# Performance work log

Hardware: AMD Instinct MI355X
Metric: run time of the kernel (lower is better)

## Reference

```python
import jax, jax.numpy as jnp
import numpy as np

B, L, T_ENC = 64, 128, 256
C_IN, UNITS, OUT = 256, 512, 128  # state_size == motor_size == UNITS (fully-connected wiring)


def _make_params(key):
    ks = jax.random.split(key, 12)
    def rn(k, shape):
        return jax.random.normal(k, shape, dtype=jnp.float32) / np.sqrt(shape[-1])
    cat = C_IN + UNITS  # CfC cell concatenates [input, hx]
    p = {}
    p["W_dec"] = rn(ks[0], (UNITS, 2 * UNITS))                 # fcn_dec, no bias
    p["W_enc"] = rn(ks[1], (UNITS, UNITS)); p["b_enc"] = jnp.zeros((UNITS,), jnp.float32)
    p["w_score"] = rn(ks[2], (1, UNITS))                       # fcn_score Linear(H,1,bias=False)
    p["W_yattn"] = rn(ks[3], (C_IN, UNITS + C_IN)); p["b_yattn"] = jnp.zeros((C_IN,), jnp.float32)
    p["W_ih"] = rn(ks[4], (4 * UNITS, C_IN)); p["b_ih"] = jnp.zeros((4 * UNITS,), jnp.float32)
    p["W_hh"] = rn(ks[5], (4 * UNITS, UNITS))                  # ncps LSTMCell recurrent map has no bias
    p["W_ff1"] = rn(ks[6], (UNITS, cat)); p["b_ff1"] = jnp.zeros((UNITS,), jnp.float32)
    p["W_ff2"] = rn(ks[7], (UNITS, cat)); p["b_ff2"] = jnp.zeros((UNITS,), jnp.float32)
    p["W_ta"] = rn(ks[8], (UNITS, cat)); p["b_ta"] = jnp.zeros((UNITS,), jnp.float32)
    p["W_tb"] = rn(ks[9], (UNITS, cat)); p["b_tb"] = jnp.zeros((UNITS,), jnp.float32)
    p["W_o1"] = rn(ks[10], (UNITS, 2 * UNITS)); p["b_o1"] = jnp.zeros((UNITS,), jnp.float32)
    p["W_o2"] = rn(ks[11], (OUT, UNITS)); p["b_o2"] = jnp.zeros((OUT,), jnp.float32)
    return p


def setup_inputs() -> dict:
    key = jax.random.key(0)
    k1, k2, k3 = jax.random.split(key, 3)
    inp = {
        "x": jax.random.normal(k1, (B, L, C_IN), dtype=jnp.float32),
        "h_en": jax.random.normal(k2, (B, T_ENC, UNITS), dtype=jnp.float32),
    }
    inp.update(_make_params(k3))
    return inp


def _forward(x, h_en, W_dec, W_enc, b_enc, w_score, W_yattn, b_yattn,
             W_ih, b_ih, W_hh, W_ff1, b_ff1, W_ff2, b_ff2,
             W_ta, b_ta, W_tb, b_tb, W_o1, b_o1, W_o2, b_o2):
    Bsz = x.shape[0]
    # fcn_enc applied once outside the time loop (as in the source)
    proj_enc = jnp.einsum('btm,hm->bth', h_en, W_enc) + b_enc  # (B,T_enc,H)
    ts = 1.0  # timespans=None

    def step(carry, xt):
        h, cst, _, _ = carry
        # attention over encoder states
        proj_dec = jnp.concatenate([h, cst], axis=1) @ W_dec.T               # (B,H)
        e = jnp.einsum('bth,h->bt', jnp.tanh(proj_dec[:, None, :] + proj_enc), w_score[0])
        score = jax.nn.softmax(e, axis=1)                                    # softmax over T_enc
        c = jnp.einsum('bt,btm->bm', score, h_en)                            # context (B,M)
        x_hat = jnp.concatenate([xt, c], axis=1) @ W_yattn.T + b_yattn       # (B,C_IN)
        # ncps LSTMCell (forget-gate bias +1)
        z = x_hat @ W_ih.T + b_ih + h @ W_hh.T
        i_, ig, fg, og = jnp.split(z, 4, axis=1)
        new_c = cst * jax.nn.sigmoid(fg + 1.0) + jnp.tanh(i_) * jax.nn.sigmoid(ig)
        h_lstm = jnp.tanh(new_c) * jax.nn.sigmoid(og)
        # WiredCfCCell: single fully-connected layer, mode='default', no backbone
        xx = jnp.concatenate([x_hat, h_lstm], axis=1)                        # (B,C_IN+H)
        ff1 = jnp.tanh(xx @ W_ff1.T + b_ff1)
        ff2 = jnp.tanh(xx @ W_ff2.T + b_ff2)
        t_interp = jax.nn.sigmoid((xx @ W_ta.T + b_ta) * ts + (xx @ W_tb.T + b_tb))
        new_h = ff1 * (1.0 - t_interp) + t_interp * ff2                      # new h_state == h_out
        return (new_h, new_c, new_h, c), None

    h0 = jnp.zeros((Bsz, UNITS), x.dtype)
    init = (h0, h0, h0, jnp.zeros((Bsz, UNITS), x.dtype))
    (h_state, c_state, h_out, c_last), _ = jax.lax.scan(step, init, jnp.swapaxes(x, 0, 1))
    hid = jax.nn.leaky_relu(jnp.concatenate([h_out, c_last], axis=1) @ W_o1.T + b_o1)
    out = hid @ W_o2.T + b_o2
    return out, h_state, c_state


def reference(x, h_en, W_dec, W_enc, b_enc, w_score, W_yattn, b_yattn,
              W_ih, b_ih, W_hh, W_ff1, b_ff1, W_ff2, b_ff2,
              W_ta, b_ta, W_tb, b_tb, W_o1, b_o1, W_o2, b_o2):
    return _forward(x, h_en, W_dec, W_enc, b_enc, w_score, W_yattn, b_yattn,
                    W_ih, b_ih, W_hh, W_ff1, b_ff1, W_ff2, b_ff2,
                    W_ta, b_ta, W_tb, b_tb, W_o1, b_o1, W_o2, b_o2)
```

## Files before the change

### kernel.cpp

```cpp
#include <hip/hip_runtime.h>


constexpr int BSZ  = 64;
constexpr int LSEQ = 128;
constexpr int TENC = 256;
constexpr int CIN  = 256;
constexpr int HU   = 512;
constexpr int ODIM = 128;
constexpr int NBLK = 256;

struct Params {
  const float *x, *h_en, *W_dec, *W_enc, *b_enc, *w_score, *W_yattn, *b_yattn;
  const float *W_ih, *b_ih, *W_hh;
  const float *W_ff1, *b_ff1, *W_ff2, *b_ff2, *W_ta, *b_ta, *W_tb, *b_tb;
  const float *W_o1, *b_o1, *W_o2, *b_o2;
  float *out;
  float *pe;
  float *pd_part;
  float *e_buf;
  float *ctx;
  float *xh_part;
  float *hlstm;
  float *h_buf;
  float *c_buf;
  float *hid;
  unsigned *bar;
  unsigned *flags;
};

__device__ __forceinline__ float frcp_(float x) { return __builtin_amdgcn_rcpf(x); }
__device__ __forceinline__ float ftanh_(float x) {
  return 1.0f - 2.0f * frcp_(1.0f + __expf(2.0f * x));
}
__device__ __forceinline__ float fsig_(float x) {
  return frcp_(1.0f + __expf(-x));
}

__device__ __forceinline__ void st_c(float* p, float v) {
  __hip_atomic_store(p, v, __ATOMIC_RELAXED, __HIP_MEMORY_SCOPE_AGENT);
}

__device__ __forceinline__ void gridbar(unsigned* bar, unsigned* flags, unsigned gen) {
  __syncthreads();
  const int t = threadIdx.x;
  if (t == 0) {
    asm volatile("s_waitcnt vmcnt(0) lgkmcnt(0)" ::: "memory");
    __hip_atomic_store(flags + blockIdx.x * 16, gen,
                       __ATOMIC_RELAXED, __HIP_MEMORY_SCOPE_AGENT);
  }
  if (blockIdx.x == 0) {
    while (__hip_atomic_load(flags + t * 16, __ATOMIC_RELAXED,
                             __HIP_MEMORY_SCOPE_AGENT) < gen)
      __builtin_amdgcn_s_sleep(1);
    __syncthreads();
    if (t == 0)
      __hip_atomic_store(bar, gen, __ATOMIC_RELAXED, __HIP_MEMORY_SCOPE_AGENT);
  }
  if (t == 0) {
    while (__hip_atomic_load(bar, __ATOMIC_RELAXED,
                             __HIP_MEMORY_SCOPE_AGENT) < gen)
      __builtin_amdgcn_s_sleep(1);
    __builtin_amdgcn_fence(__ATOMIC_ACQUIRE, "agent");
  }
  __syncthreads();
}

__device__ __forceinline__ void dot2x2(const float* A0, const float* A1,
                                       const float* W0, const float* W1,
                                       int nk4, float (&acc)[2][2]) {
#pragma unroll 8
  for (int k4 = 0; k4 < nk4; ++k4) {
    float4 w0 = *(const float4*)(W0 + (k4 << 2));
    float4 w1 = *(const float4*)(W1 + (k4 << 2));
    float4 a0 = *(const float4*)(A0 + (k4 << 2));
    float4 a1 = *(const float4*)(A1 + (k4 << 2));
    acc[0][0] = fmaf(a0.x, w0.x, acc[0][0]); acc[0][0] = fmaf(a0.y, w0.y, acc[0][0]);
    acc[0][0] = fmaf(a0.z, w0.z, acc[0][0]); acc[0][0] = fmaf(a0.w, w0.w, acc[0][0]);
    acc[0][1] = fmaf(a0.x, w1.x, acc[0][1]); acc[0][1] = fmaf(a0.y, w1.y, acc[0][1]);
    acc[0][1] = fmaf(a0.z, w1.z, acc[0][1]); acc[0][1] = fmaf(a0.w, w1.w, acc[0][1]);
    acc[1][0] = fmaf(a1.x, w0.x, acc[1][0]); acc[1][0] = fmaf(a1.y, w0.y, acc[1][0]);
    acc[1][0] = fmaf(a1.z, w0.z, acc[1][0]); acc[1][0] = fmaf(a1.w, w0.w, acc[1][0]);
    acc[1][1] = fmaf(a1.x, w1.x, acc[1][1]); acc[1][1] = fmaf(a1.y, w1.y, acc[1][1]);
    acc[1][1] = fmaf(a1.z, w1.z, acc[1][1]); acc[1][1] = fmaf(a1.w, w1.w, acc[1][1]);
  }
}

__device__ __forceinline__ void dot1x2(const float* A0,
                                       const float* W0, const float* W1,
                                       int nk4, float (&acc)[2]) {
#pragma unroll 8
  for (int k4 = 0; k4 < nk4; ++k4) {
    float4 w0 = *(const float4*)(W0 + (k4 << 2));
    float4 w1 = *(const float4*)(W1 + (k4 << 2));
    float4 a  = *(const float4*)(A0 + (k4 << 2));
    acc[0] = fmaf(a.x, w0.x, acc[0]); acc[0] = fmaf(a.y, w0.y, acc[0]);
    acc[0] = fmaf(a.z, w0.z, acc[0]); acc[0] = fmaf(a.w, w0.w, acc[0]);
    acc[1] = fmaf(a.x, w1.x, acc[1]); acc[1] = fmaf(a.y, w1.y, acc[1]);
    acc[1] = fmaf(a.z, w1.z, acc[1]); acc[1] = fmaf(a.w, w1.w, acc[1]);
  }
}

__device__ __forceinline__ void dot2x4(const float* A0, const float* A1,
                                       const float* W0, const float* W1,
                                       const float* W2, const float* W3,
                                       int nk4, float (&acc)[2][4]) {
#pragma unroll 4
  for (int k4 = 0; k4 < nk4; ++k4) {
    float4 w0 = *(const float4*)(W0 + (k4 << 2));
    float4 w1 = *(const float4*)(W1 + (k4 << 2));
    float4 w2 = *(const float4*)(W2 + (k4 << 2));
    float4 w3 = *(const float4*)(W3 + (k4 << 2));
#pragma unroll
    for (int i = 0; i < 2; ++i) {
      float4 a = *(const float4*)((i ? A1 : A0) + (k4 << 2));
      acc[i][0] = fmaf(a.x, w0.x, acc[i][0]); acc[i][0] = fmaf(a.y, w0.y, acc[i][0]);
      acc[i][0] = fmaf(a.z, w0.z, acc[i][0]); acc[i][0] = fmaf(a.w, w0.w, acc[i][0]);
      acc[i][1] = fmaf(a.x, w1.x, acc[i][1]); acc[i][1] = fmaf(a.y, w1.y, acc[i][1]);
      acc[i][1] = fmaf(a.z, w1.z, acc[i][1]); acc[i][1] = fmaf(a.w, w1.w, acc[i][1]);
      acc[i][2] = fmaf(a.x, w2.x, acc[i][2]); acc[i][2] = fmaf(a.y, w2.y, acc[i][2]);
      acc[i][2] = fmaf(a.z, w2.z, acc[i][2]); acc[i][2] = fmaf(a.w, w2.w, acc[i][2]);
      acc[i][3] = fmaf(a.x, w3.x, acc[i][3]); acc[i][3] = fmaf(a.y, w3.y, acc[i][3]);
      acc[i][3] = fmaf(a.z, w3.z, acc[i][3]); acc[i][3] = fmaf(a.w, w3.w, acc[i][3]);
    }
  }
}

__launch_bounds__(256)
__global__ void cfc_kernel(Params P) {
  __shared__ float lds[12800];
  __shared__ const float* wrA[32];
  __shared__ const float* wrB[32];
  __shared__ float biasS[32];

  const int t = threadIdx.x;
  unsigned gen = 1;

  for (int job = blockIdx.x; job < 4096 + 32; job += NBLK) {
    if (job < 4096) {
      int rt = job & 255, ct = job >> 8;
      if (t < 32) {
        wrA[t] = P.W_enc + (ct * 32 + t) * HU;
        biasS[t] = P.b_enc[ct * 32 + t];
      }
      const int c0 = (t & 7) * 4, b0 = (t >> 3) * 2;
      __syncthreads();
      float acc[2][4];
#pragma unroll
      for (int i = 0; i < 2; ++i)
#pragma unroll
        for (int j = 0; j < 4; ++j) acc[i][j] = biasS[c0 + j];
      const float* Ab = P.h_en + (size_t)(rt * 64) * HU;
      for (int s = 0; s < 4; ++s) {
        int ko = s * 128;
        for (int idx = t; idx < 2048; idx += 256) {
          int r = idx >> 5, c4 = idx & 31;
          *(float4*)&lds[r * 132 + (c4 << 2)] =
            *(const float4*)(Ab + (size_t)r * HU + ko + (c4 << 2));
        }
        for (int idx = t; idx < 1024; idx += 256) {
          int r = idx >> 5, c4 = idx & 31;
          *(float4*)&lds[8448 + r * 132 + (c4 << 2)] =
            *(const float4*)(wrA[r] + ko + (c4 << 2));
        }
        __syncthreads();
        dot2x4(&lds[b0 * 132], &lds[(b0 + 1) * 132],
               &lds[8448 + c0 * 132], &lds[8448 + (c0 + 1) * 132],
               &lds[8448 + (c0 + 2) * 132], &lds[8448 + (c0 + 3) * 132], 32, acc);
        __syncthreads();
      }
      float* outp = P.pe + (size_t)(rt * 64) * HU + ct * 32;
#pragma unroll
      for (int i = 0; i < 2; ++i)
#pragma unroll
        for (int j = 0; j < 4; ++j)
          outp[(b0 + i) * HU + c0 + j] = acc[i][j];
    } else {
      int idx = job - 4096;
      float* base = (idx < 16 ? P.h_buf : P.c_buf) + (idx & 15) * 2048;
      for (int i = t; i < 2048; i += 256) st_c(base + i, 0.f);
    }
  }
  __builtin_amdgcn_fence(__ATOMIC_RELEASE, "agent");
  gridbar(P.bar, P.flags, gen++);

  for (int step = 0; step < LSEQ; ++step) {

    {
      int ut = blockIdx.x & 31, ks = blockIdx.x >> 5;
      if (t < 16) wrA[t] = P.W_dec + (ut * 16 + t) * 1024 + ks * 128;
      const int c0 = (t & 7) * 2, b0 = (t >> 3) * 2;
      const float* Asrc = (ks < 4) ? (P.h_buf + ks * 128) : (P.c_buf + (ks - 4) * 128);
      __syncthreads();
      float acc[2][2] = {{0.f, 0.f}, {0.f, 0.f}};
      for (int idx = t; idx < 2048; idx += 256) {
        int r = idx >> 5, c4 = idx & 31;
        *(float4*)&lds[r * 132 + (c4 << 2)] =
          *(const float4*)(Asrc + r * HU + (c4 << 2));
      }
      for (int idx = t; idx < 512; idx += 256) {
        int r = idx >> 5, c4 = idx & 31;
        *(float4*)&lds[8448 + r * 132 + (c4 << 2)] =
          *(const float4*)(wrA[r] + (c4 << 2));
      }
      __syncthreads();
      dot2x2(&lds[b0 * 132], &lds[(b0 + 1) * 132],
             &lds[8448 + c0 * 132], &lds[8448 + (c0 + 1) * 132], 32, acc);
      float* outp = P.pd_part + ks * (BSZ * HU) + ut * 16;
      st_c(outp + b0 * HU + c0,           acc[0][0]);
      st_c(outp + b0 * HU + c0 + 1,       acc[0][1]);
      st_c(outp + (b0 + 1) * HU + c0,     acc[1][0]);
      st_c(outp + (b0 + 1) * HU + c0 + 1, acc[1][1]);
    }
    gridbar(P.bar, P.flags, gen++);

    {
      int b = blockIdx.x >> 2, tq = blockIdx.x & 3;
      float* pds = lds;
      float* wsc = lds + 520;
      __syncthreads();
      {
        int h = t * 2;
        float sx = 0.f, sy = 0.f;
#pragma unroll
        for (int p8 = 0; p8 < 8; ++p8) {
          float2 v = *(const float2*)(P.pd_part + p8 * (BSZ * HU) + b * HU + h);
          sx += v.x; sy += v.y;
        }
        int hs = h + (h >> 7);
        pds[hs] = sx; pds[hs + 1] = sy;
        float2 w = *(const float2*)(P.w_score + h);
        wsc[hs] = w.x; wsc[hs + 1] = w.y;
      }
      __syncthreads();
      int q = t & 3, tt = tq * 64 + (t >> 2);
      const float* per = P.pe + (size_t)(b * TENC + tt) * HU + q * 128;
      const float* pd = pds + q * 129;
      const float* wv = wsc + q * 129;
      float acc = 0.f;
      for (int h4 = 0; h4 < 32; ++h4) {
        float4 pv = *(const float4*)(per + (h4 << 2));
        int o = h4 << 2;
        acc += wv[o + 0] * ftanh_(pd[o + 0] + pv.x);
        acc += wv[o + 1] * ftanh_(pd[o + 1] + pv.y);
        acc += wv[o + 2] * ftanh_(pd[o + 2] + pv.z);
        acc += wv[o + 3] * ftanh_(pd[o + 3] + pv.w);
      }
      acc += __shfl_xor(acc, 1);
      acc += __shfl_xor(acc, 2);
      if (q == 0) st_c(P.e_buf + b * TENC + tt, acc);
    }
    gridbar(P.bar, P.flags, gen++);

    {
      int b = blockIdx.x >> 2, mq = blockIdx.x & 3;
      float* es = lds;
      float* red = lds + 260;
      float v = P.e_buf[b * TENC + t];
      float m = v;
#pragma unroll
      for (int o = 1; o < 64; o <<= 1) m = fmaxf(m, __shfl_xor(m, o));
      int wid = t >> 6;
      if ((t & 63) == 0) red[wid] = m;
      __syncthreads();
      m = fmaxf(fmaxf(red[0], red[1]), fmaxf(red[2], red[3]));
      float p = __expf(v - m);
      float s = p;
#pragma unroll
      for (int o = 1; o < 64; o <<= 1) s += __shfl_xor(s, o);
      if ((t & 63) == 0) red[4 + wid] = s;
      __syncthreads();
      float sum = (red[4] + red[5]) + (red[6] + red[7]);
      es[t] = p * frcp_(sum);
      __syncthreads();
      if (t < 128) {
        int mcol = mq * 128 + t;
        const float* hb = P.h_en + (size_t)b * TENC * HU + mcol;
        float a0 = 0.f, a1 = 0.f, a2 = 0.f, a3 = 0.f;
        for (int tt = 0; tt < TENC; tt += 4) {
          a0 = fmaf(es[tt + 0], hb[(tt + 0) * HU], a0);
          a1 = fmaf(es[tt + 1], hb[(tt + 1) * HU], a1);
          a2 = fmaf(es[tt + 2], hb[(tt + 2) * HU], a2);
          a3 = fmaf(es[tt + 3], hb[(tt + 3) * HU], a3);
        }
        st_c(P.ctx + b * HU + mcol, (a0 + a1) + (a2 + a3));
      }
    }
    gridbar(P.bar, P.flags, gen++);

    if (blockIdx.x < 32) {
      int ct = blockIdx.x & 15, ks = blockIdx.x >> 4;
      if (t < 16) {
        wrA[t] = P.W_yattn + (ct * 16 + t) * 768 + ks * 384;
        biasS[t] = ks ? 0.f : P.b_yattn[ct * 16 + t];
      }
      const int c0 = (t & 7) * 2, b0 = (t >> 3) * 2;
      __syncthreads();
      float acc[2][2];
      acc[0][0] = biasS[c0]; acc[0][1] = biasS[c0 + 1];
      acc[1][0] = biasS[c0]; acc[1][1] = biasS[c0 + 1];
      for (int s = 0; s < 3; ++s) {
        int k = ks * 384 + s * 128;
        for (int idx = t; idx < 2048; idx += 256) {
          int r = idx >> 5, c4 = idx & 31;
          const float* src = (k < 256)
            ? (P.x + ((size_t)r * LSEQ + step) * CIN + k)
            : (P.ctx + r * HU + (k - 256));
          *(float4*)&lds[r * 132 + (c4 << 2)] = *(const float4*)(src + (c4 << 2));
        }
        for (int idx = t; idx < 512; idx += 256) {
          int r = idx >> 5, c4 = idx & 31;
          *(float4*)&lds[8448 + r * 132 + (c4 << 2)] =
            *(const float4*)(wrA[r] + s * 128 + (c4 << 2));
        }
        __syncthreads();
        dot2x2(&lds[b0 * 132], &lds[(b0 + 1) * 132],
               &lds[8448 + c0 * 132], &lds[8448 + (c0 + 1) * 132], 32, acc);
        __syncthreads();
      }
      float* outp = P.xh_part + ks * (BSZ * CIN) + ct * 16;
      st_c(outp + b0 * CIN + c0,           acc[0][0]);
      st_c(outp + b0 * CIN + c0 + 1,       acc[0][1]);
      st_c(outp + (b0 + 1) * CIN + c0,     acc[1][0]);
      st_c(outp + (b0 + 1) * CIN + c0 + 1, acc[1][1]);
    }
    gridbar(P.bar, P.flags, gen++);

    {
      int bt = blockIdx.x & 1, jq = blockIdx.x >> 1;
      int j0 = jq * 4, rowbase = bt * 32;
      if (t < 16) {
        int jj = t >> 2, g = t & 3;
        int r = g * 512 + j0 + jj;
        wrA[t] = P.W_ih + r * 256;
        wrB[t] = P.W_hh + (size_t)r * 512;
        biasS[t] = P.b_ih[r];
      }
      const int c0 = (t & 7) * 2, b0 = t >> 3;
      __syncthreads();
      float acc[2];
      acc[0] = biasS[c0]; acc[1] = biasS[c0 + 1];
      for (int s = 0; s < 3; ++s) {
        if (s == 0) {
          for (int idx = t; idx < 2048; idx += 256) {
            int r = idx >> 6, c4 = idx & 63; int gb = rowbase + r;
            float4 a = *(const float4*)(P.xh_part + gb * CIN + (c4 << 2));
            float4 b2 = *(const float4*)(P.xh_part + BSZ * CIN + gb * CIN + (c4 << 2));
            a.x += b2.x; a.y += b2.y; a.z += b2.z; a.w += b2.w;
            *(float4*)&lds[r * 260 + (c4 << 2)] = a;
          }
          for (int idx = t; idx < 1024; idx += 256) {
            int r = idx >> 6, c4 = idx & 63;
            *(float4*)&lds[8320 + r * 260 + (c4 << 2)] =
              *(const float4*)(wrA[r] + (c4 << 2));
          }
        } else {
          int ho = (s - 1) * 256;
          for (int idx = t; idx < 2048; idx += 256) {
            int r = idx >> 6, c4 = idx & 63; int gb = rowbase + r;
            *(float4*)&lds[r * 260 + (c4 << 2)] =
              *(const float4*)(P.h_buf + gb * HU + ho + (c4 << 2));
          }
          for (int idx = t; idx < 1024; idx += 256) {
            int r = idx >> 6, c4 = idx & 63;
            *(float4*)&lds[8320 + r * 260 + (c4 << 2)] =
              *(const float4*)(wrB[r] + ho + (c4 << 2));
          }
        }
        __syncthreads();
        dot1x2(&lds[b0 * 260], &lds[8320 + c0 * 260], &lds[8320 + (c0 + 1) * 260], 64, acc);
        __syncthreads();
      }
      float* zs = lds;
      zs[b0 * 16 + c0] = acc[0];
      zs[b0 * 16 + c0 + 1] = acc[1];
      __syncthreads();
      if (t < 128) {
        int b2 = t >> 2, jj = t & 3;
        int gb = rowbase + b2, j = j0 + jj;
        float i_ = zs[b2 * 16 + jj * 4 + 0];
        float ig = zs[b2 * 16 + jj * 4 + 1];
        float fg = zs[b2 * 16 + jj * 4 + 2];
        float og = zs[b2 * 16 + jj * 4 + 3];
        float cold = P.c_buf[gb * HU + j];
        float cn = cold * fsig_(fg + 1.0f) + ftanh_(i_) * fsig_(ig);
        st_c(P.c_buf + gb * HU + j, cn);
        st_c(P.hlstm + gb * HU + j, ftanh_(cn) * fsig_(og));
      }
    }
    gridbar(P.bar, P.flags, gen++);

    {
      int bt = blockIdx.x & 1, jq = blockIdx.x >> 1;
      int j0 = jq * 4, rowbase = bt * 32;
      if (t < 16) {
        int jj = t >> 2, m = t & 3;
        const float* Wm = (m == 0) ? P.W_ff1 : (m == 1) ? P.W_ff2 : (m == 2) ? P.W_ta : P.W_tb;
        const float* bm = (m == 0) ? P.b_ff1 : (m == 1) ? P.b_ff2 : (m == 2) ? P.b_ta : P.b_tb;
        wrA[t] = Wm + (j0 + jj) * 768;
        biasS[t] = bm[j0 + jj];
      }
      const int c0 = (t & 7) * 2, b0 = t >> 3;
      __syncthreads();
      float acc[2];
      acc[0] = biasS[c0]; acc[1] = biasS[c0 + 1];
      for (int s = 0; s < 3; ++s) {
        if (s == 0) {
          for (int idx = t; idx < 2048; idx += 256) {
            int r = idx >> 6, c4 = idx & 63; int gb = rowbase + r;
            float4 a = *(const float4*)(P.xh_part + gb * CIN + (c4 << 2));
            float4 b2 = *(const float4*)(P.xh_part + BSZ * CIN + gb * CIN + (c4 << 2));
            a.x += b2.x; a.y += b2.y; a.z += b2.z; a.w += b2.w;
            *(float4*)&lds[r * 260 + (c4 << 2)] = a;
          }
        } else {
          int ho = (s - 1) * 256;
          for (int idx = t; idx < 2048; idx += 256) {
            int r = idx >> 6, c4 = idx & 63; int gb = rowbase + r;
            *(float4*)&lds[r * 260 + (c4 << 2)] =
              *(const float4*)(P.hlstm + gb * HU + ho + (c4 << 2));
          }
        }
        for (int idx = t; idx < 1024; idx += 256) {
          int r = idx >> 6, c4 = idx & 63;
          *(float4*)&lds[8320 + r * 260 + (c4 << 2)] =
            *(const float4*)(wrA[r] + s * 256 + (c4 << 2));
        }
        __syncthreads();
        dot1x2(&lds[b0 * 260], &lds[8320 + c0 * 260], &lds[8320 + (c0 + 1) * 260], 64, acc);
        __syncthreads();
      }
      float* es2 = lds;
      es2[b0 * 16 + c0] = acc[0];
      es2[b0 * 16 + c0 + 1] = acc[1];
      __syncthreads();
      if (t < 128) {
        int b2 = t >> 2, jj = t & 3;
        int gb = rowbase + b2, j = j0 + jj;
        float ff1 = ftanh_(es2[b2 * 16 + jj * 4 + 0]);
        float ff2 = ftanh_(es2[b2 * 16 + jj * 4 + 1]);
        float ta  = es2[b2 * 16 + jj * 4 + 2];
        float tb  = es2[b2 * 16 + jj * 4 + 3];
        float ti = fsig_(ta + tb);
        st_c(P.h_buf + gb * HU + j, ff1 * (1.0f - ti) + ti * ff2);
      }
    }
    gridbar(P.bar, P.flags, gen++);
  }

  if (blockIdx.x < 64) {
    int bt = blockIdx.x & 1, ut = blockIdx.x >> 1;
    int rowbase = bt * 32;
    if (t < 16) {
      wrA[t] = P.W_o1 + (ut * 16 + t) * 1024;
      biasS[t] = P.b_o1[ut * 16 + t];
    }
    const int c0 = (t & 7) * 2, b0 = t >> 3;
    __syncthreads();
    float acc[2];
    acc[0] = biasS[c0]; acc[1] = biasS[c0 + 1];
    for (int s = 0; s < 4; ++s) {
      const float* src = (s < 2) ? (P.h_buf + s * 256) : (P.ctx + (s - 2) * 256);
      for (int idx = t; idx < 2048; idx += 256) {
        int r = idx >> 6, c4 = idx & 63; int gb = rowbase + r;
        *(float4*)&lds[r * 260 + (c4 << 2)] = *(const float4*)(src + gb * HU + (c4 << 2));
      }
      for (int idx = t; idx < 1024; idx += 256) {
        int r = idx >> 6, c4 = idx & 63;
        *(float4*)&lds[8320 + r * 260 + (c4 << 2)] =
          *(const float4*)(wrA[r] + s * 256 + (c4 << 2));
      }
      __syncthreads();
      dot1x2(&lds[b0 * 260], &lds[8320 + c0 * 260], &lds[8320 + (c0 + 1) * 260], 64, acc);
      __syncthreads();
    }
#pragma unroll
    for (int j = 0; j < 2; ++j) {
      float v = acc[j];
      st_c(P.hid + (rowbase + b0) * HU + ut * 16 + c0 + j, v > 0.f ? v : 0.01f * v);
    }
  }
  gridbar(P.bar, P.flags, gen++);

  {
    int job = blockIdx.x;
    if (job < 16) {
      int bt = job & 1, ot = job >> 1;
      int rowbase = bt * 32;
      if (t < 16) {
        wrA[t] = P.W_o2 + (ot * 16 + t) * HU;
        biasS[t] = P.b_o2[ot * 16 + t];
      }
      const int c0 = (t & 7) * 2, b0 = t >> 3;
      __syncthreads();
      float acc[2];
      acc[0] = biasS[c0]; acc[1] = biasS[c0 + 1];
      for (int s = 0; s < 2; ++s) {
        for (int idx = t; idx < 2048; idx += 256) {
          int r = idx >> 6, c4 = idx & 63; int gb = rowbase + r;
          *(float4*)&lds[r * 260 + (c4 << 2)] =
            *(const float4*)(P.hid + gb * HU + s * 256 + (c4 << 2));
        }
        for (int idx = t; idx < 1024; idx += 256) {
          int r = idx >> 6, c4 = idx & 63;
          *(float4*)&lds[8320 + r * 260 + (c4 << 2)] =
            *(const float4*)(wrA[r] + s * 256 + (c4 << 2));
        }
        __syncthreads();
        dot1x2(&lds[b0 * 260], &lds[8320 + c0 * 260], &lds[8320 + (c0 + 1) * 260], 64, acc);
        __syncthreads();
      }
      P.out[(rowbase + b0) * ODIM + ot * 16 + c0]     = acc[0];
      P.out[(rowbase + b0) * ODIM + ot * 16 + c0 + 1] = acc[1];
    } else if (job < 48) {
      int idx = job - 16;
      const float* src = (idx < 16 ? P.h_buf : P.c_buf) + (idx & 15) * 2048;
      float* dst = P.out + BSZ * ODIM + (idx < 16 ? 0 : BSZ * HU) + (idx & 15) * 2048;
      for (int i = t; i < 512; i += 256)
        *(float4*)(dst + 4 * i) = *(const float4*)(src + 4 * i);
    }
  }
}

extern "C" void kernel_launch(void* const* d_in, const int* in_sizes, int n_in,
                              void* d_out, int out_size, void* d_ws, size_t ws_size,
                              hipStream_t stream) {
  (void)in_sizes; (void)n_in; (void)out_size; (void)ws_size;
  Params P;
  P.x       = (const float*)d_in[0];
  P.h_en    = (const float*)d_in[1];
  P.W_dec   = (const float*)d_in[2];
  P.W_enc   = (const float*)d_in[3];
  P.b_enc   = (const float*)d_in[4];
  P.w_score = (const float*)d_in[5];
  P.W_yattn = (const float*)d_in[6];
  P.b_yattn = (const float*)d_in[7];
  P.W_ih    = (const float*)d_in[8];
  P.b_ih    = (const float*)d_in[9];
  P.W_hh    = (const float*)d_in[10];
  P.W_ff1   = (const float*)d_in[11];
  P.b_ff1   = (const float*)d_in[12];
  P.W_ff2   = (const float*)d_in[13];
  P.b_ff2   = (const float*)d_in[14];
  P.W_ta    = (const float*)d_in[15];
  P.b_ta    = (const float*)d_in[16];
  P.W_tb    = (const float*)d_in[17];
  P.b_tb    = (const float*)d_in[18];
  P.W_o1    = (const float*)d_in[19];
  P.b_o1    = (const float*)d_in[20];
  P.W_o2    = (const float*)d_in[21];
  P.b_o2    = (const float*)d_in[22];
  P.out     = (float*)d_out;

  float* ws = (float*)d_ws;
  size_t off = 0;
  P.pe      = ws + off; off += (size_t)BSZ * TENC * HU;
  P.pd_part = ws + off; off += (size_t)8 * BSZ * HU;
  P.e_buf   = ws + off; off += (size_t)BSZ * TENC;
  P.ctx     = ws + off; off += (size_t)BSZ * HU;
  P.xh_part = ws + off; off += (size_t)2 * BSZ * CIN;
  P.hlstm   = ws + off; off += (size_t)BSZ * HU;
  P.h_buf   = ws + off; off += (size_t)BSZ * HU;
  P.c_buf   = ws + off; off += (size_t)BSZ * HU;
  P.hid     = ws + off; off += (size_t)BSZ * HU;
  P.bar     = (unsigned*)(ws + off); off += 16;
  P.flags   = (unsigned*)(ws + off);

  (void)hipMemsetAsync((void*)P.bar, 0, 64 + 256 * 64, stream);

  hipLaunchKernelGGL(cfc_kernel, dim3(NBLK), dim3(256), 0, stream, P);
}
```

Before: 14.44 ms.

## Read weights directly from global memory and use coherent sc1 loads instead of acquire fences

Weight tiles are no longer staged into LDS. The dot-product helpers now read weight rows straight from global memory (L2/L1), and only activations go through LDS. The acquire fence after the grid barrier is removed. Cross-block activation reads now use inline-asm global_load_dwordx4 with sc1, or relaxed agent-scope atomic loads, so the loads see other blocks' writes without a cache invalidate at each barrier. This is meant to cut LDS traffic and the per-barrier fence cost in the recurrent loop, but it depends on the sc1 bit giving the needed coherence on this architecture and replaces LDS reads with uncoalesced per-thread global weight reads.

```diff
diff --git a/kernel.cpp b/kernel.cpp
--- a/kernel.cpp
+++ b/kernel.cpp
@@ -8,6 +8,9 @@
 constexpr int HU   = 512;
 constexpr int ODIM = 128;
 constexpr int NBLK = 256;
+
+typedef float f32x4 __attribute__((ext_vector_type(4)));
+typedef unsigned long long ull;
 
 struct Params {
   const float *x, *h_en, *W_dec, *W_enc, *b_enc, *w_score, *W_yattn, *b_yattn;
@@ -39,6 +42,33 @@
 __device__ __forceinline__ void st_c(float* p, float v) {
   __hip_atomic_store(p, v, __ATOMIC_RELAXED, __HIP_MEMORY_SCOPE_AGENT);
 }
+__device__ __forceinline__ float ld_a(const float* p) {
+  return __hip_atomic_load(p, __ATOMIC_RELAXED, __HIP_MEMORY_SCOPE_AGENT);
+}
+__device__ __forceinline__ float2 ld_a2(const float* p) {
+  union { ull u; float2 f; } c;
+  c.u = __hip_atomic_load((const ull*)p, __ATOMIC_RELAXED, __HIP_MEMORY_SCOPE_AGENT);
+  return c.f;
+}
+
+__device__ __forceinline__ void sc1_ld8(const float* const (&p)[8], f32x4 (&v)[8]) {
+  asm volatile(
+    "global_load_dwordx4 %0, %8, off sc1\n\t"
+    "global_load_dwordx4 %1, %9, off sc1\n\t"
+    "global_load_dwordx4 %2, %10, off sc1\n\t"
+    "global_load_dwordx4 %3, %11, off sc1\n\t"
+    "global_load_dwordx4 %4, %12, off sc1\n\t"
+    "global_load_dwordx4 %5, %13, off sc1\n\t"
+    "global_load_dwordx4 %6, %14, off sc1\n\t"
+    "global_load_dwordx4 %7, %15, off sc1\n\t"
+    "s_waitcnt vmcnt(0)"
+    : "=&v"(v[0]), "=&v"(v[1]), "=&v"(v[2]), "=&v"(v[3]),
+      "=&v"(v[4]), "=&v"(v[5]), "=&v"(v[6]), "=&v"(v[7])
+    : "v"(p[0]), "v"(p[1]), "v"(p[2]), "v"(p[3]),
+      "v"(p[4]), "v"(p[5]), "v"(p[6]), "v"(p[7])
+    : "memory");
+  __builtin_amdgcn_sched_barrier(0);
+}
 
 __device__ __forceinline__ void gridbar(unsigned* bar, unsigned* flags, unsigned gen) {
   __syncthreads();
@@ -60,14 +90,13 @@
     while (__hip_atomic_load(bar, __ATOMIC_RELAXED,
                              __HIP_MEMORY_SCOPE_AGENT) < gen)
       __builtin_amdgcn_s_sleep(1);
-    __builtin_amdgcn_fence(__ATOMIC_ACQUIRE, "agent");
   }
   __syncthreads();
 }
 
-__device__ __forceinline__ void dot2x2(const float* A0, const float* A1,
-                                       const float* W0, const float* W1,
-                                       int nk4, float (&acc)[2][2]) {
+__device__ __forceinline__ void dotg2x2(const float* A0, const float* A1,
+                                        const float* W0, const float* W1,
+                                        int nk4, float (&acc)[2][2]) {
 #pragma unroll 8
   for (int k4 = 0; k4 < nk4; ++k4) {
     float4 w0 = *(const float4*)(W0 + (k4 << 2));
@@ -85,9 +114,9 @@
   }
 }
 
-__device__ __forceinline__ void dot1x2(const float* A0,
-                                       const float* W0, const float* W1,
-                                       int nk4, float (&acc)[2]) {
+__device__ __forceinline__ void dotg1x2(const float* A0,
+                                        const float* W0, const float* W1,
+                                        int nk4, float (&acc)[2]) {
 #pragma unroll 8
   for (int k4 = 0; k4 < nk4; ++k4) {
     float4 w0 = *(const float4*)(W0 + (k4 << 2));
@@ -100,10 +129,10 @@
   }
 }
 
-__device__ __forceinline__ void dot2x4(const float* A0, const float* A1,
-                                       const float* W0, const float* W1,
-                                       const float* W2, const float* W3,
-                                       int nk4, float (&acc)[2][4]) {
+__device__ __forceinline__ void dotg2x4(const float* A0, const float* A1,
+                                        const float* W0, const float* W1,
+                                        const float* W2, const float* W3,
+                                        int nk4, float (&acc)[2][4]) {
 #pragma unroll 4
   for (int k4 = 0; k4 < nk4; ++k4) {
     float4 w0 = *(const float4*)(W0 + (k4 << 2));
@@ -127,9 +156,9 @@
 
 __launch_bounds__(256)
 __global__ void cfc_kernel(Params P) {
-  __shared__ float lds[12800];
+  __shared__ float lds[8448];
   __shared__ const float* wrA[32];
-  __shared__ const float* wrB[32];
+  __shared__ const float* wrB[16];
   __shared__ float biasS[32];
 
   const int t = threadIdx.x;
@@ -150,22 +179,18 @@
 #pragma unroll
         for (int j = 0; j < 4; ++j) acc[i][j] = biasS[c0 + j];
       const float* Ab = P.h_en + (size_t)(rt * 64) * HU;
+      const float* W0 = wrA[c0], *W1 = wrA[c0 + 1], *W2 = wrA[c0 + 2], *W3 = wrA[c0 + 3];
       for (int s = 0; s < 4; ++s) {
         int ko = s * 128;
-        for (int idx = t; idx < 2048; idx += 256) {
-          int r = idx >> 5, c4 = idx & 31;
+#pragma unroll
+        for (int i = 0; i < 8; ++i) {
+          int idx = t + i * 256; int r = idx >> 5, c4 = idx & 31;
           *(float4*)&lds[r * 132 + (c4 << 2)] =
             *(const float4*)(Ab + (size_t)r * HU + ko + (c4 << 2));
         }
-        for (int idx = t; idx < 1024; idx += 256) {
-          int r = idx >> 5, c4 = idx & 31;
-          *(float4*)&lds[8448 + r * 132 + (c4 << 2)] =
-            *(const float4*)(wrA[r] + ko + (c4 << 2));
-        }
-        __syncthreads();
-        dot2x4(&lds[b0 * 132], &lds[(b0 + 1) * 132],
-               &lds[8448 + c0 * 132], &lds[8448 + (c0 + 1) * 132],
-               &lds[8448 + (c0 + 2) * 132], &lds[8448 + (c0 + 3) * 132], 32, acc);
+        __syncthreads();
+        dotg2x4(&lds[b0 * 132], &lds[(b0 + 1) * 132],
+                W0 + ko, W1 + ko, W2 + ko, W3 + ko, 32, acc);
         __syncthreads();
       }
       float* outp = P.pe + (size_t)(rt * 64) * HU + ct * 32;
@@ -191,20 +216,23 @@
       const int c0 = (t & 7) * 2, b0 = (t >> 3) * 2;
       const float* Asrc = (ks < 4) ? (P.h_buf + ks * 128) : (P.c_buf + (ks - 4) * 128);
       __syncthreads();
+      {
+        const float* p[8]; f32x4 v[8];
+#pragma unroll
+        for (int i = 0; i < 8; ++i) {
+          int idx = t + i * 256; int r = idx >> 5, c4 = idx & 31;
+          p[i] = Asrc + r * HU + (c4 << 2);
+        }
+        sc1_ld8(p, v);
+#pragma unroll
+        for (int i = 0; i < 8; ++i) {
+          int idx = t + i * 256; int r = idx >> 5, c4 = idx & 31;
+          *(f32x4*)&lds[r * 132 + (c4 << 2)] = v[i];
+        }
+      }
+      __syncthreads();
       float acc[2][2] = {{0.f, 0.f}, {0.f, 0.f}};
-      for (int idx = t; idx < 2048; idx += 256) {
-        int r = idx >> 5, c4 = idx & 31;
-        *(float4*)&lds[r * 132 + (c4 << 2)] =
-          *(const float4*)(Asrc + r * HU + (c4 << 2));
-      }
-      for (int idx = t; idx < 512; idx += 256) {
-        int r = idx >> 5, c4 = idx & 31;
-        *(float4*)&lds[8448 + r * 132 + (c4 << 2)] =
-          *(const float4*)(wrA[r] + (c4 << 2));
-      }
-      __syncthreads();
-      dot2x2(&lds[b0 * 132], &lds[(b0 + 1) * 132],
-             &lds[8448 + c0 * 132], &lds[8448 + (c0 + 1) * 132], 32, acc);
+      dotg2x2(&lds[b0 * 132], &lds[(b0 + 1) * 132], wrA[c0], wrA[c0 + 1], 32, acc);
       float* outp = P.pd_part + ks * (BSZ * HU) + ut * 16;
       st_c(outp + b0 * HU + c0,           acc[0][0]);
       st_c(outp + b0 * HU + c0 + 1,       acc[0][1]);
@@ -223,7 +251,7 @@
         float sx = 0.f, sy = 0.f;
 #pragma unroll
         for (int p8 = 0; p8 < 8; ++p8) {
-          float2 v = *(const float2*)(P.pd_part + p8 * (BSZ * HU) + b * HU + h);
+          float2 v = ld_a2(P.pd_part + p8 * (BSZ * HU) + b * HU + h);
           sx += v.x; sy += v.y;
         }
         int hs = h + (h >> 7);
@@ -255,7 +283,7 @@
       int b = blockIdx.x >> 2, mq = blockIdx.x & 3;
       float* es = lds;
       float* red = lds + 260;
-      float v = P.e_buf[b * TENC + t];
+      float v = ld_a(P.e_buf + b * TENC + t);
       float m = v;
 #pragma unroll
       for (int o = 1; o < 64; o <<= 1) m = fmaxf(m, __shfl_xor(m, o));
@@ -298,23 +326,33 @@
       float acc[2][2];
       acc[0][0] = biasS[c0]; acc[0][1] = biasS[c0 + 1];
       acc[1][0] = biasS[c0]; acc[1][1] = biasS[c0 + 1];
+      const float* W0 = wrA[c0], *W1 = wrA[c0 + 1];
       for (int s = 0; s < 3; ++s) {
         int k = ks * 384 + s * 128;
-        for (int idx = t; idx < 2048; idx += 256) {
-          int r = idx >> 5, c4 = idx & 31;
-          const float* src = (k < 256)
-            ? (P.x + ((size_t)r * LSEQ + step) * CIN + k)
-            : (P.ctx + r * HU + (k - 256));
-          *(float4*)&lds[r * 132 + (c4 << 2)] = *(const float4*)(src + (c4 << 2));
-        }
-        for (int idx = t; idx < 512; idx += 256) {
-          int r = idx >> 5, c4 = idx & 31;
-          *(float4*)&lds[8448 + r * 132 + (c4 << 2)] =
-            *(const float4*)(wrA[r] + s * 128 + (c4 << 2));
-        }
-        __syncthreads();
-        dot2x2(&lds[b0 * 132], &lds[(b0 + 1) * 132],
-               &lds[8448 + c0 * 132], &lds[8448 + (c0 + 1) * 132], 32, acc);
+        if (k < 256) {
+#pragma unroll
+          for (int i = 0; i < 8; ++i) {
+            int idx = t + i * 256; int r = idx >> 5, c4 = idx & 31;
+            *(float4*)&lds[r * 132 + (c4 << 2)] =
+              *(const float4*)(P.x + ((size_t)r * LSEQ + step) * CIN + k + (c4 << 2));
+          }
+        } else {
+          const float* p[8]; f32x4 v[8];
+#pragma unroll
+          for (int i = 0; i < 8; ++i) {
+            int idx = t + i * 256; int r = idx >> 5, c4 = idx & 31;
+            p[i] = P.ctx + r * HU + (k - 256) + (c4 << 2);
+          }
+          sc1_ld8(p, v);
+#pragma unroll
+          for (int i = 0; i < 8; ++i) {
+            int idx = t + i * 256; int r = idx >> 5, c4 = idx & 31;
+            *(f32x4*)&lds[r * 132 + (c4 << 2)] = v[i];
+          }
+        }
+        __syncthreads();
+        dotg2x2(&lds[b0 * 132], &lds[(b0 + 1) * 132],
+                W0 + s * 128, W1 + s * 128, 32, acc);
         __syncthreads();
       }
       float* outp = P.xh_part + ks * (BSZ * CIN) + ct * 16;
@@ -341,33 +379,40 @@
       acc[0] = biasS[c0]; acc[1] = biasS[c0 + 1];
       for (int s = 0; s < 3; ++s) {
         if (s == 0) {
-          for (int idx = t; idx < 2048; idx += 256) {
-            int r = idx >> 6, c4 = idx & 63; int gb = rowbase + r;
-            float4 a = *(const float4*)(P.xh_part + gb * CIN + (c4 << 2));
-            float4 b2 = *(const float4*)(P.xh_part + BSZ * CIN + gb * CIN + (c4 << 2));
-            a.x += b2.x; a.y += b2.y; a.z += b2.z; a.w += b2.w;
-            *(float4*)&lds[r * 260 + (c4 << 2)] = a;
-          }
-          for (int idx = t; idx < 1024; idx += 256) {
-            int r = idx >> 6, c4 = idx & 63;
-            *(float4*)&lds[8320 + r * 260 + (c4 << 2)] =
-              *(const float4*)(wrA[r] + (c4 << 2));
+          const float* p[8]; f32x4 v[8], v2[8];
+#pragma unroll
+          for (int i = 0; i < 8; ++i) {
+            int idx = t + i * 256; int r = idx >> 6, c4 = idx & 63;
+            p[i] = P.xh_part + (rowbase + r) * CIN + (c4 << 2);
+          }
+          sc1_ld8(p, v);
+#pragma unroll
+          for (int i = 0; i < 8; ++i) p[i] += BSZ * CIN;
+          sc1_ld8(p, v2);
+#pragma unroll
+          for (int i = 0; i < 8; ++i) {
+            int idx = t + i * 256; int r = idx >> 6, c4 = idx & 63;
+            *(f32x4*)&lds[r * 260 + (c4 << 2)] = v[i] + v2[i];
           }
         } else {
           int ho = (s - 1) * 256;
-          for (int idx = t; idx < 2048; idx += 256) {
-            int r = idx >> 6, c4 = idx & 63; int gb = rowbase + r;
-            *(float4*)&lds[r * 260 + (c4 << 2)] =
-              *(const float4*)(P.h_buf + gb * HU + ho + (c4 << 2));
-          }
-          for (int idx = t; idx < 1024; idx += 256) {
-            int r = idx >> 6, c4 = idx & 63;
-            *(float4*)&lds[8320 + r * 260 + (c4 << 2)] =
-              *(const float4*)(wrB[r] + ho + (c4 << 2));
-          }
-        }
-        __syncthreads();
-        dot1x2(&lds[b0 * 260], &lds[8320 + c0 * 260], &lds[8320 + (c0 + 1) * 260], 64, acc);
+          const float* p[8]; f32x4 v[8];
+#pragma unroll
+          for (int i = 0; i < 8; ++i) {
+            int idx = t + i * 256; int r = idx >> 6, c4 = idx & 63;
+            p[i] = P.h_buf + (rowbase + r) * HU + ho + (c4 << 2);
+          }
+          sc1_ld8(p, v);
+#pragma unroll
+          for (int i = 0; i < 8; ++i) {
+            int idx = t + i * 256; int r = idx >> 6, c4 = idx & 63;
+            *(f32x4*)&lds[r * 260 + (c4 << 2)] = v[i];
+          }
+        }
+        __syncthreads();
+        const float* W0 = (s == 0) ? wrA[c0]     : wrB[c0] + (s - 1) * 256;
+        const float* W1 = (s == 0) ? wrA[c0 + 1] : wrB[c0 + 1] + (s - 1) * 256;
+        dotg1x2(&lds[b0 * 260], W0, W1, 64, acc);
         __syncthreads();
       }
       float* zs = lds;
@@ -381,7 +426,7 @@
         float ig = zs[b2 * 16 + jj * 4 + 1];
         float fg = zs[b2 * 16 + jj * 4 + 2];
         float og = zs[b2 * 16 + jj * 4 + 3];
-        float cold = P.c_buf[gb * HU + j];
+        float cold = ld_a(P.c_buf + gb * HU + j);
         float cn = cold * fsig_(fg + 1.0f) + ftanh_(i_) * fsig_(ig);
         st_c(P.c_buf + gb * HU + j, cn);
         st_c(P.hlstm + gb * HU + j, ftanh_(cn) * fsig_(og));
@@ -405,28 +450,38 @@
       acc[0] = biasS[c0]; acc[1] = biasS[c0 + 1];
       for (int s = 0; s < 3; ++s) {
         if (s == 0) {
-          for (int idx = t; idx < 2048; idx += 256) {
-            int r = idx >> 6, c4 = idx & 63; int gb = rowbase + r;
-            float4 a = *(const float4*)(P.xh_part + gb * CIN + (c4 << 2));
-            float4 b2 = *(const float4*)(P.xh_part + BSZ * CIN + gb * CIN + (c4 << 2));
-            a.x += b2.x; a.y += b2.y; a.z += b2.z; a.w += b2.w;
-            *(float4*)&lds[r * 260 + (c4 << 2)] = a;
+          const float* p[8]; f32x4 v[8], v2[8];
+#pragma unroll
+          for (int i = 0; i < 8; ++i) {
+            int idx = t + i * 256; int r = idx >> 6, c4 = idx & 63;
+            p[i] = P.xh_part + (rowbase + r) * CIN + (c4 << 2);
+          }
+          sc1_ld8(p, v);
+#pragma unroll
+          for (int i = 0; i < 8; ++i) p[i] += BSZ * CIN;
+          sc1_ld8(p, v2);
+#pragma unroll
+          for (int i = 0; i < 8; ++i) {
+            int idx = t + i * 256; int r = idx >> 6, c4 = idx & 63;
+            *(f32x4*)&lds[r * 260 + (c4 << 2)] = v[i] + v2[i];
           }
         } else {
           int ho = (s - 1) * 256;
-          for (int idx = t; idx < 2048; idx += 256) {
-            int r = idx >> 6, c4 = idx & 63; int gb = rowbase + r;
-            *(float4*)&lds[r * 260 + (c4 << 2)] =
-              *(const float4*)(P.hlstm + gb * HU + ho + (c4 << 2));
-          }
-        }
-        for (int idx = t; idx < 1024; idx += 256) {
-          int r = idx >> 6, c4 = idx & 63;
-          *(float4*)&lds[8320 + r * 260 + (c4 << 2)] =
-            *(const float4*)(wrA[r] + s * 256 + (c4 << 2));
-        }
-        __syncthreads();
-        dot1x2(&lds[b0 * 260], &lds[8320 + c0 * 260], &lds[8320 + (c0 + 1) * 260], 64, acc);
+          const float* p[8]; f32x4 v[8];
+#pragma unroll
+          for (int i = 0; i < 8; ++i) {
+            int idx = t + i * 256; int r = idx >> 6, c4 = idx & 63;
+            p[i] = P.hlstm + (rowbase + r) * HU + ho + (c4 << 2);
+          }
+          sc1_ld8(p, v);
+#pragma unroll
+          for (int i = 0; i < 8; ++i) {
+            int idx = t + i * 256; int r = idx >> 6, c4 = idx & 63;
+            *(f32x4*)&lds[r * 260 + (c4 << 2)] = v[i];
+          }
+        }
+        __syncthreads();
+        dotg1x2(&lds[b0 * 260], wrA[c0] + s * 256, wrA[c0 + 1] + s * 256, 64, acc);
         __syncthreads();
       }
       float* es2 = lds;
@@ -460,23 +515,26 @@
     acc[0] = biasS[c0]; acc[1] = biasS[c0 + 1];
     for (int s = 0; s < 4; ++s) {
       const float* src = (s < 2) ? (P.h_buf + s * 256) : (P.ctx + (s - 2) * 256);
-      for (int idx = t; idx < 2048; idx += 256) {
-        int r = idx >> 6, c4 = idx & 63; int gb = rowbase + r;
-        *(float4*)&lds[r * 260 + (c4 << 2)] = *(const float4*)(src + gb * HU + (c4 << 2));
-      }
-      for (int idx = t; idx < 1024; idx += 256) {
-        int r = idx >> 6, c4 = idx & 63;
-        *(float4*)&lds[8320 + r * 260 + (c4 << 2)] =
-          *(const float4*)(wrA[r] + s * 256 + (c4 << 2));
-      }
-      __syncthreads();
-      dot1x2(&lds[b0 * 260], &lds[8320 + c0 * 260], &lds[8320 + (c0 + 1) * 260], 64, acc);
+      const float* p[8]; f32x4 v[8];
+#pragma unroll
+      for (int i = 0; i < 8; ++i) {
+        int idx = t + i * 256; int r = idx >> 6, c4 = idx & 63;
+        p[i] = src + (rowbase + r) * HU + (c4 << 2);
+      }
+      sc1_ld8(p, v);
+#pragma unroll
+      for (int i = 0; i < 8; ++i) {
+        int idx = t + i * 256; int r = idx >> 6, c4 = idx & 63;
+        *(f32x4*)&lds[r * 260 + (c4 << 2)] = v[i];
+      }
+      __syncthreads();
+      dotg1x2(&lds[b0 * 260], wrA[c0] + s * 256, wrA[c0 + 1] + s * 256, 64, acc);
       __syncthreads();
     }
 #pragma unroll
     for (int j = 0; j < 2; ++j) {
-      float v = acc[j];
-      st_c(P.hid + (rowbase + b0) * HU + ut * 16 + c0 + j, v > 0.f ? v : 0.01f * v);
+      float v2 = acc[j];
+      st_c(P.hid + (rowbase + b0) * HU + ut * 16 + c0 + j, v2 > 0.f ? v2 : 0.01f * v2);
     }
   }
   gridbar(P.bar, P.flags, gen++);
@@ -495,18 +553,20 @@
       float acc[2];
       acc[0] = biasS[c0]; acc[1] = biasS[c0 + 1];
       for (int s = 0; s < 2; ++s) {
-        for (int idx = t; idx < 2048; idx += 256) {
-          int r = idx >> 6, c4 = idx & 63; int gb = rowbase + r;
-          *(float4*)&lds[r * 260 + (c4 << 2)] =
-            *(const float4*)(P.hid + gb * HU + s * 256 + (c4 << 2));
-        }
-        for (int idx = t; idx < 1024; idx += 256) {
-          int r = idx >> 6, c4 = idx & 63;
-          *(float4*)&lds[8320 + r * 260 + (c4 << 2)] =
-            *(const float4*)(wrA[r] + s * 256 + (c4 << 2));
-        }
-        __syncthreads();
-        dot1x2(&lds[b0 * 260], &lds[8320 + c0 * 260], &lds[8320 + (c0 + 1) * 260], 64, acc);
+        const float* p[8]; f32x4 v[8];
+#pragma unroll
+        for (int i = 0; i < 8; ++i) {
+          int idx = t + i * 256; int r = idx >> 6, c4 = idx & 63;
+          p[i] = P.hid + (rowbase + r) * HU + s * 256 + (c4 << 2);
+        }
+        sc1_ld8(p, v);
+#pragma unroll
+        for (int i = 0; i < 8; ++i) {
+          int idx = t + i * 256; int r = idx >> 6, c4 = idx & 63;
+          *(f32x4*)&lds[r * 260 + (c4 << 2)] = v[i];
+        }
+        __syncthreads();
+        dotg1x2(&lds[b0 * 260], wrA[c0] + s * 256, wrA[c0 + 1] + s * 256, 64, acc);
         __syncthreads();
       }
       P.out[(rowbase + b0) * ODIM + ot * 16 + c0]     = acc[0];
@@ -515,8 +575,14 @@
       int idx = job - 16;
       const float* src = (idx < 16 ? P.h_buf : P.c_buf) + (idx & 15) * 2048;
       float* dst = P.out + BSZ * ODIM + (idx < 16 ? 0 : BSZ * HU) + (idx & 15) * 2048;
-      for (int i = t; i < 512; i += 256)
-        *(float4*)(dst + 4 * i) = *(const float4*)(src + 4 * i);
+      for (int i = t; i < 512; i += 256) {
+        const float* p[8]; f32x4 v[8];
+        (void)p; (void)v;
+      }
+      for (int i = t; i < 1024; i += 256) {
+        float2 f = ld_a2(src + 2 * i);
+        *(float2*)(dst + 2 * i) = f;
+      }
     }
   }
 }
```

Result: slower. 23.48 ms (+62.6%).
